# Kernel optimization log

Measured on AMD Instinct MI355X. Metric: run time of the kernel, lower is better.

## Reference

```python
import jax, jax.numpy as jnp
import numpy as np

B, T, C, H = 4, 4096, 1024, 64

def setup_inputs() -> dict:
    key = jax.random.key(0)
    kx, kk, kq, kv = jax.random.split(key, 4)
    x = jax.random.normal(kx, (B, T, C), dtype=jnp.float32)
    # causal lower-triangular mask; masked_fill where mask == 0
    mask = jnp.tril(jnp.ones((T, T), dtype=jnp.int32))
    s = 1.0 / np.sqrt(C)
    Wk = jax.random.normal(kk, (H, C), dtype=jnp.float32) * s
    Wq = jax.random.normal(kq, (H, C), dtype=jnp.float32) * s
    Wv = jax.random.normal(kv, (H, C), dtype=jnp.float32) * s
    return {"x": x, "mask": mask, "Wk": Wk, "Wq": Wq, "Wv": Wv}

def reference(x, mask, Wk, Wq, Wv):
    # single-head attention; dropout is identity in eval mode
    scale = Wk.shape[0] ** -0.5  # head_size ** -0.5
    k = jnp.einsum('btc,hc->bth', x, Wk)  # [B,T,H]
    q = jnp.einsum('btc,hc->bth', x, Wq)
    v = jnp.einsum('btc,hc->bth', x, Wv)
    att = jnp.einsum('bqh,bkh->bqk', q, k) * scale  # [B,T,T]
    att = jnp.where(mask == 0, -jnp.inf, att)
    att = jax.nn.softmax(att, axis=-1)
    out = jnp.einsum('bqk,bkh->bqh', att, v)  # [B,T,H]
    return out
```

## Files before the change

kernel.cpp:

```cpp
#include <hip/hip_runtime.h>
#include <hip/hip_bf16.h>

#define BT 16384
#define CDIM 1024
#define HD 64
#define TT 4096

typedef __bf16 bf16x8 __attribute__((ext_vector_type(8)));
typedef __bf16 bf16x4 __attribute__((ext_vector_type(4)));
typedef float f32x4 __attribute__((ext_vector_type(4)));

__device__ __forceinline__ f32x4 mfma16(bf16x8 a, bf16x8 b, f32x4 c){
  return __builtin_amdgcn_mfma_f32_16x16x32_bf16(a, b, c, 0, 0, 0);
}

__device__ __forceinline__ void glds16(const __bf16* g, __bf16* l){
  __builtin_amdgcn_global_load_lds(
      (const __attribute__((address_space(1))) unsigned int*)g,
      (__attribute__((address_space(3))) unsigned int*)l, 16, 0, 0);
}

__global__ __launch_bounds__(256) void wconv_k(const float* __restrict__ Wk,
    const float* __restrict__ Wq, const float* __restrict__ Wv,
    __bf16* __restrict__ Wbf){
  int idx = blockIdx.x*256 + threadIdx.x;
  int e0 = idx*4;
  int n = e0 >> 10;
  int c = e0 & 1023;
  const float* src; float s;
  if (n < 64)      { src = Wk + (size_t)n*CDIM;       s = 1.0f;   }
  else if (n < 128){ src = Wq + (size_t)(n-64)*CDIM;  s = 0.125f; }
  else             { src = Wv + (size_t)(n-128)*CDIM; s = 1.0f;   }
  float4 v = *reinterpret_cast<const float4*>(src + c);
  __bf16* dst = Wbf + e0;
  dst[0]=(__bf16)(v.x*s); dst[1]=(__bf16)(v.y*s);
  dst[2]=(__bf16)(v.z*s); dst[3]=(__bf16)(v.w*s);
}

__global__ __launch_bounds__(256) void proj_k(const float* __restrict__ x,
    const __bf16* __restrict__ Wbf, __bf16* __restrict__ kb,
    __bf16* __restrict__ qb, __bf16* __restrict__ vTb){
  __shared__ __bf16 Wt[2][192*64];
  __shared__ __bf16 Xt[2][32*64];

  const int tid  = threadIdx.x;
  const int lane = tid & 63;
  const int w    = tid >> 6;
  const int wr   = w >> 1;
  const int wn   = w & 1;
  const int l15  = lane & 15, g = lane >> 4;
  const long row0 = (long)blockIdx.x*32;

  const int xrw  = tid >> 3, xc16 = tid & 7;
  const float* xsrc = x + (row0 + xrw)*CDIM + xc16*8;
  const int    xdst = xrw*64 + ((xc16 ^ (xrw & 7))*8);

  const int swz0 = ((g    ) ^ (l15 & 7))*8;
  const int swz1 = ((g + 4) ^ (l15 & 7))*8;

  f32x4 acc[6];
  #pragma unroll
  for (int j=0;j<6;j++) acc[j] = (f32x4)(0.0f);

  float4 xlo, xhi;

  #pragma unroll
  for (int j=0;j<6;j++){
    const int s  = j*256 + w*64 + lane;
    const int rw = s >> 3, c16 = s & 7;
    glds16(Wbf + (size_t)rw*CDIM + ((c16 ^ (rw & 7))*8),
           &Wt[0][(j*256 + w*64)*8]);
  }
  xlo = *reinterpret_cast<const float4*>(xsrc);
  xhi = *reinterpret_cast<const float4*>(xsrc + 4);
  {
    bf16x8 xv;
    xv[0]=(__bf16)xlo.x; xv[1]=(__bf16)xlo.y; xv[2]=(__bf16)xlo.z; xv[3]=(__bf16)xlo.w;
    xv[4]=(__bf16)xhi.x; xv[5]=(__bf16)xhi.y; xv[6]=(__bf16)xhi.z; xv[7]=(__bf16)xhi.w;
    *reinterpret_cast<bf16x8*>(&Xt[0][xdst]) = xv;
  }
  xlo = *reinterpret_cast<const float4*>(xsrc + 64);
  xhi = *reinterpret_cast<const float4*>(xsrc + 64 + 4);
  asm volatile("s_waitcnt lgkmcnt(0)" ::: "memory");
  __builtin_amdgcn_sched_barrier(0);
  __builtin_amdgcn_s_barrier();
  __builtin_amdgcn_sched_barrier(0);

  #pragma unroll
  for (int t=0; t<16; ++t){
    const int cur = t & 1, nxt = cur ^ 1;

    if (t+1 < 16){
      const int kk0 = (t+1)*64;
      #pragma unroll
      for (int j=0;j<6;j++){
        const int s  = j*256 + w*64 + lane;
        const int rw = s >> 3, c16 = s & 7;
        glds16(Wbf + (size_t)rw*CDIM + kk0 + ((c16 ^ (rw & 7))*8),
               &Wt[nxt][(j*256 + w*64)*8]);
      }
    }
    if (t+1 < 16){
      bf16x8 xv;
      xv[0]=(__bf16)xlo.x; xv[1]=(__bf16)xlo.y; xv[2]=(__bf16)xlo.z; xv[3]=(__bf16)xlo.w;
      xv[4]=(__bf16)xhi.x; xv[5]=(__bf16)xhi.y; xv[6]=(__bf16)xhi.z; xv[7]=(__bf16)xhi.w;
      *reinterpret_cast<bf16x8*>(&Xt[nxt][xdst]) = xv;
    }
    if (t+2 < 16){
      const int nk = (t+2)*64;
      xlo = *reinterpret_cast<const float4*>(xsrc + nk);
      xhi = *reinterpret_cast<const float4*>(xsrc + nk + 4);
    }
    {
      const __bf16* ab = &Xt[cur][(wr*16 + l15)*64];
      bf16x8 a0 = *reinterpret_cast<const bf16x8*>(ab + swz0);
      bf16x8 a1 = *reinterpret_cast<const bf16x8*>(ab + swz1);
      const __bf16* bb = &Wt[cur][(wn*96 + l15)*64];
      #pragma unroll
      for (int nf=0; nf<6; ++nf){
        bf16x8 b0 = *reinterpret_cast<const bf16x8*>(bb + nf*1024 + swz0);
        bf16x8 b1 = *reinterpret_cast<const bf16x8*>(bb + nf*1024 + swz1);
        acc[nf] = mfma16(a1, b1, mfma16(a0, b0, acc[nf]));
      }
    }
    if (t+1 < 16){
      if (t+2 < 16){
        asm volatile("s_waitcnt vmcnt(2)" ::: "memory");
      } else {
        asm volatile("s_waitcnt vmcnt(0)" ::: "memory");
      }
      asm volatile("s_waitcnt lgkmcnt(0)" ::: "memory");
      __builtin_amdgcn_sched_barrier(0);
      __builtin_amdgcn_s_barrier();
      __builtin_amdgcn_sched_barrier(0);
    }
  }

  const long bidx = row0 >> 12;
  #pragma unroll
  for (int nf=0;nf<6;nf++){
    const int n0  = wn*96 + nf*16 + l15;
    const int mat = n0 >> 6;
    const int h   = n0 & 63;
    const long rbase = row0 + wr*16 + g*4;
    if (mat == 0){
      #pragma unroll
      for (int r=0;r<4;r++) kb[(rbase+r)*HD + h] = (__bf16)acc[nf][r];
    } else if (mat == 1){
      #pragma unroll
      for (int r=0;r<4;r++) qb[(rbase+r)*HD + h] = (__bf16)acc[nf][r];
    } else {
      bf16x4 t4;
      #pragma unroll
      for (int r=0;r<4;r++) t4[r] = (__bf16)acc[nf][r];
      *reinterpret_cast<bf16x4*>(vTb + (bidx*64 + h)*TT + (rbase & 4095)) = t4;
    }
  }
}

template<int NS>
__global__ __launch_bounds__(256) void attn_part_k(const __bf16* __restrict__ kbg,
    const __bf16* __restrict__ qbg, const __bf16* __restrict__ vT,
    __bf16* __restrict__ po, float* __restrict__ pl){
  __shared__ __bf16 Klds[64][72];
  __shared__ __bf16 Vlds[64][72];
  __shared__ __bf16 Plds[4][16][72];

  const int tid  = threadIdx.x;
  const int lane = tid & 63;
  const int w    = tid >> 6;
  const int l15  = lane & 15, g = lane >> 4;

  const int bi  = blockIdx.x;
  const int b   = bi / (64*NS);
  const int rem = bi % (64*NS);
  const int qt  = 63 - rem / NS;
  const int s   = rem % NS;

  const int ntiles = qt + 1;
  const int lo = ( s      * ntiles) / NS;
  const int hi = ((s + 1) * ntiles) / NS;
  const int pidx = (b*64 + qt)*NS + s;

  if (lo == hi){
    if (l15 == 0){
      #pragma unroll
      for (int r=0;r<4;r++) pl[pidx*64 + w*16 + g*4 + r] = 0.0f;
    }
    return;
  }

  const long qbase = (long)b*TT + (long)qt*64;

  bf16x8 qf0, qf1;
  {
    const __bf16* src = qbg + (qbase + w*16 + l15)*HD + g*8;
    qf0 = *reinterpret_cast<const bf16x8*>(src);
    qf1 = *reinterpret_cast<const bf16x8*>(src + 32);
  }

  f32x4 o[4];
  #pragma unroll
  for (int ch=0; ch<4; ++ch) o[ch] = (f32x4)(0.0f);
  float lp[4] = {0.f, 0.f, 0.f, 0.f};

  const __bf16* vbase = vT + (size_t)b*64*TT;

  const int skey = tid >> 2;
  const int sd0  = (tid & 3) * 16;
  bf16x8 kr0, kr1, vr0, vr1;

  {
    const long kvbase = (long)b*TT + (long)lo*64;
    const __bf16* ks = kbg + (kvbase + skey)*HD + sd0;
    kr0 = *reinterpret_cast<const bf16x8*>(ks);
    kr1 = *reinterpret_cast<const bf16x8*>(ks+8);
    const __bf16* vs = vbase + (size_t)skey*TT + lo*64 + sd0;
    vr0 = *reinterpret_cast<const bf16x8*>(vs);
    vr1 = *reinterpret_cast<const bf16x8*>(vs+8);
  }

  for (int kv=lo; kv<hi; ++kv){
    __syncthreads();
    *reinterpret_cast<bf16x8*>(&Klds[skey][sd0])   = kr0;
    *reinterpret_cast<bf16x8*>(&Klds[skey][sd0+8]) = kr1;
    *reinterpret_cast<bf16x8*>(&Vlds[skey][sd0])   = vr0;
    *reinterpret_cast<bf16x8*>(&Vlds[skey][sd0+8]) = vr1;
    __syncthreads();

    if (kv+1 < hi){
      const long nbase = (long)b*TT + (long)(kv+1)*64;
      const __bf16* ks = kbg + (nbase + skey)*HD + sd0;
      kr0 = *reinterpret_cast<const bf16x8*>(ks);
      kr1 = *reinterpret_cast<const bf16x8*>(ks+8);
      const __bf16* vs = vbase + (size_t)skey*TT + (kv+1)*64 + sd0;
      vr0 = *reinterpret_cast<const bf16x8*>(vs);
      vr1 = *reinterpret_cast<const bf16x8*>(vs+8);
    }

    f32x4 sv[4];
    __builtin_amdgcn_s_setprio(1);
    #pragma unroll
    for (int c=0;c<4;c++){
      bf16x8 kb0 = *reinterpret_cast<const bf16x8*>(&Klds[c*16 + l15][g*8]);
      bf16x8 kb1 = *reinterpret_cast<const bf16x8*>(&Klds[c*16 + l15][g*8 + 32]);
      sv[c] = mfma16(qf0, kb0, (f32x4)(-16.0f));
      sv[c] = mfma16(qf1, kb1, sv[c]);
    }
    __builtin_amdgcn_s_setprio(0);

    if (kv == qt){
      #pragma unroll
      for (int c=0;c<4;c++){
        const int key = c*16 + l15;
        #pragma unroll
        for (int r=0;r<4;r++){
          const int qr = w*16 + g*4 + r;
          if (key > qr) sv[c][r] = -1e30f;
        }
      }
    }

    #pragma unroll
    for (int c=0;c<4;c++){
      #pragma unroll
      for (int r=0;r<4;r++) sv[c][r] = __expf(sv[c][r]);
    }
    #pragma unroll
    for (int r=0;r<4;r++)
      lp[r] += (sv[0][r] + sv[1][r]) + (sv[2][r] + sv[3][r]);

    #pragma unroll
    for (int c=0;c<4;c++){
      #pragma unroll
      for (int r=0;r<4;r++) Plds[w][g*4+r][c*16 + l15] = (__bf16)sv[c][r];
    }
    asm volatile("s_waitcnt lgkmcnt(0)" ::: "memory");
    __builtin_amdgcn_sched_barrier(0);
    bf16x8 pa0 = *reinterpret_cast<const bf16x8*>(&Plds[w][l15][g*8]);
    bf16x8 pa1 = *reinterpret_cast<const bf16x8*>(&Plds[w][l15][g*8 + 32]);

    __builtin_amdgcn_s_setprio(1);
    #pragma unroll
    for (int ch=0; ch<4; ++ch){
      bf16x8 vb0 = *reinterpret_cast<const bf16x8*>(&Vlds[ch*16 + l15][g*8]);
      bf16x8 vb1 = *reinterpret_cast<const bf16x8*>(&Vlds[ch*16 + l15][g*8 + 32]);
      o[ch] = mfma16(pa0, vb0, o[ch]);
      o[ch] = mfma16(pa1, vb1, o[ch]);
    }
    __builtin_amdgcn_s_setprio(0);
  }

  float lr[4];
  #pragma unroll
  for (int r=0;r<4;r++){
    float v = lp[r];
    v += __shfl_xor(v, 1);
    v += __shfl_xor(v, 2);
    v += __shfl_xor(v, 4);
    v += __shfl_xor(v, 8);
    lr[r] = v;
  }
  float rl[4];
  #pragma unroll
  for (int r=0;r<4;r++) rl[r] = (lr[r] > 0.0f) ? 1.0f/lr[r] : 0.0f;

  __bf16* podst = po + (size_t)pidx*4096;
  #pragma unroll
  for (int ch=0; ch<4; ++ch){
    #pragma unroll
    for (int r=0;r<4;r++)
      podst[(w*16 + g*4 + r)*64 + ch*16 + l15] = (__bf16)(o[ch][r] * rl[r]);
  }
  if (l15 == 0){
    #pragma unroll
    for (int r=0;r<4;r++) pl[pidx*64 + w*16 + g*4 + r] = lr[r];
  }
}

template<int NS>
__global__ __launch_bounds__(256) void comb_k(const __bf16* __restrict__ po,
    const float* __restrict__ pl, float* __restrict__ out){
  const int idx   = blockIdx.x*256 + threadIdx.x;
  const int qrow  = idx >> 6;
  const int dim   = idx & 63;
  const int qtg   = qrow >> 6;
  const int rowin = qrow & 63;

  float num = 0.0f, den = 0.0f;
  #pragma unroll
  for (int s=0;s<NS;s++){
    const float l = pl[(qtg*NS + s)*64 + rowin];
    den += l;
    num += l * (float)po[(size_t)(qtg*NS + s)*4096 + rowin*64 + dim];
  }
  out[idx] = num / den;
}

extern "C" void kernel_launch(void* const* d_in, const int* in_sizes, int n_in,
                              void* d_out, int out_size, void* d_ws, size_t ws_size,
                              hipStream_t stream) {
  const float* x  = (const float*)d_in[0];
  const float* Wk = (const float*)d_in[2];
  const float* Wq = (const float*)d_in[3];
  const float* Wv = (const float*)d_in[4];
  float* out = (float*)d_out;

  char* ws = (char*)d_ws;
  __bf16* Wbf = (__bf16*)ws;
  __bf16* kb  = (__bf16*)(ws + 393216);
  __bf16* qb  = (__bf16*)(ws + 2490368);
  __bf16* vTb = (__bf16*)(ws + 4587520);
  __bf16* po  = (__bf16*)(ws + 6684672);

  wconv_k<<<192, 256, 0, stream>>>(Wk, Wq, Wv, Wbf);
  proj_k <<<512, 256, 0, stream>>>(x, Wbf, kb, qb, vTb);

  const size_t need8 = 6684672ull + (size_t)2048*4096*2 + (size_t)2048*64*4;
  if (ws_size >= need8){
    float* pl = (float*)(ws + 6684672 + (size_t)2048*4096*2);
    attn_part_k<8><<<2048, 256, 0, stream>>>(kb, qb, vTb, po, pl);
    comb_k<8>    <<<4096, 256, 0, stream>>>(po, pl, out);
  } else {
    float* pl = (float*)(ws + 6684672 + (size_t)1024*4096*2);
    attn_part_k<4><<<1024, 256, 0, stream>>>(kb, qb, vTb, po, pl);
    comb_k<4>    <<<4096, 256, 0, stream>>>(po, pl, out);
  }
}
```

Measured before the change: 62.60 us.

## Widen attention blocks to 128 query rows with 8 waves sharing K/V tiles

The split-KV attention kernel now processes 128 query rows per block with 512 threads (8 waves), so each K/V tile loaded into LDS is reused by twice as many query rows. The split count drops to a fixed 4, with 512 blocks in place of 2048. Waves whose rows lie entirely above a key tile skip it, and the diagonal mask is generalized. The combine kernel and workspace layout are adapted to match. This halves K/V global traffic per query row but reduces the number of blocks and adds causal imbalance across waves within a block.

```diff
diff --git a/kernel.cpp b/kernel.cpp
--- a/kernel.cpp
+++ b/kernel.cpp
@@ -5,6 +5,7 @@
 #define CDIM 1024
 #define HD 64
 #define TT 4096
+#define NS2 4
 
 typedef __bf16 bf16x8 __attribute__((ext_vector_type(8)));
 typedef __bf16 bf16x4 __attribute__((ext_vector_type(4)));
@@ -158,13 +159,12 @@
   }
 }
 
-template<int NS>
-__global__ __launch_bounds__(256) void attn_part_k(const __bf16* __restrict__ kbg,
+__global__ __launch_bounds__(512) void attn_part_k(const __bf16* __restrict__ kbg,
     const __bf16* __restrict__ qbg, const __bf16* __restrict__ vT,
     __bf16* __restrict__ po, float* __restrict__ pl){
   __shared__ __bf16 Klds[64][72];
   __shared__ __bf16 Vlds[64][72];
-  __shared__ __bf16 Plds[4][16][72];
+  __shared__ __bf16 Plds[8][16][72];
 
   const int tid  = threadIdx.x;
   const int lane = tid & 63;
@@ -172,25 +172,25 @@
   const int l15  = lane & 15, g = lane >> 4;
 
   const int bi  = blockIdx.x;
-  const int b   = bi / (64*NS);
-  const int rem = bi % (64*NS);
-  const int qt  = 63 - rem / NS;
-  const int s   = rem % NS;
-
-  const int ntiles = qt + 1;
-  const int lo = ( s      * ntiles) / NS;
-  const int hi = ((s + 1) * ntiles) / NS;
-  const int pidx = (b*64 + qt)*NS + s;
+  const int b   = bi / (32*NS2);
+  const int rem = bi % (32*NS2);
+  const int qt  = 31 - rem / NS2;
+  const int s   = rem % NS2;
+
+  const int ntiles = 2*qt + 2;
+  const int lo = ( s      * ntiles) / NS2;
+  const int hi = ((s + 1) * ntiles) / NS2;
+  const int pidx = (b*32 + qt)*NS2 + s;
 
   if (lo == hi){
     if (l15 == 0){
       #pragma unroll
-      for (int r=0;r<4;r++) pl[pidx*64 + w*16 + g*4 + r] = 0.0f;
+      for (int r=0;r<4;r++) pl[pidx*128 + w*16 + g*4 + r] = 0.0f;
     }
     return;
   }
 
-  const long qbase = (long)b*TT + (long)qt*64;
+  const long qbase = (long)b*TT + (long)qt*128;
 
   bf16x8 qf0, qf1;
   {
@@ -206,37 +206,30 @@
 
   const __bf16* vbase = vT + (size_t)b*64*TT;
 
-  const int skey = tid >> 2;
-  const int sd0  = (tid & 3) * 16;
-  bf16x8 kr0, kr1, vr0, vr1;
+  const int skey = tid >> 3;
+  const int sd0  = (tid & 7) * 8;
+  bf16x8 kr, vr;
 
   {
     const long kvbase = (long)b*TT + (long)lo*64;
-    const __bf16* ks = kbg + (kvbase + skey)*HD + sd0;
-    kr0 = *reinterpret_cast<const bf16x8*>(ks);
-    kr1 = *reinterpret_cast<const bf16x8*>(ks+8);
-    const __bf16* vs = vbase + (size_t)skey*TT + lo*64 + sd0;
-    vr0 = *reinterpret_cast<const bf16x8*>(vs);
-    vr1 = *reinterpret_cast<const bf16x8*>(vs+8);
+    kr = *reinterpret_cast<const bf16x8*>(kbg + (kvbase + skey)*HD + sd0);
+    vr = *reinterpret_cast<const bf16x8*>(vbase + (size_t)skey*TT + lo*64 + sd0);
   }
 
   for (int kv=lo; kv<hi; ++kv){
     __syncthreads();
-    *reinterpret_cast<bf16x8*>(&Klds[skey][sd0])   = kr0;
-    *reinterpret_cast<bf16x8*>(&Klds[skey][sd0+8]) = kr1;
-    *reinterpret_cast<bf16x8*>(&Vlds[skey][sd0])   = vr0;
-    *reinterpret_cast<bf16x8*>(&Vlds[skey][sd0+8]) = vr1;
+    *reinterpret_cast<bf16x8*>(&Klds[skey][sd0]) = kr;
+    *reinterpret_cast<bf16x8*>(&Vlds[skey][sd0]) = vr;
     __syncthreads();
 
     if (kv+1 < hi){
       const long nbase = (long)b*TT + (long)(kv+1)*64;
-      const __bf16* ks = kbg + (nbase + skey)*HD + sd0;
-      kr0 = *reinterpret_cast<const bf16x8*>(ks);
-      kr1 = *reinterpret_cast<const bf16x8*>(ks+8);
-      const __bf16* vs = vbase + (size_t)skey*TT + (kv+1)*64 + sd0;
-      vr0 = *reinterpret_cast<const bf16x8*>(vs);
-      vr1 = *reinterpret_cast<const bf16x8*>(vs+8);
-    }
+      kr = *reinterpret_cast<const bf16x8*>(kbg + (nbase + skey)*HD + sd0);
+      vr = *reinterpret_cast<const bf16x8*>(vbase + (size_t)skey*TT + (kv+1)*64 + sd0);
+    }
+
+    const int kk0 = kv*64 - qt*128;
+    if (kk0 > w*16 + 15) continue;
 
     f32x4 sv[4];
     __builtin_amdgcn_s_setprio(1);
@@ -249,14 +242,14 @@
     }
     __builtin_amdgcn_s_setprio(0);
 
-    if (kv == qt){
+    if (kk0 + 63 > w*16){
       #pragma unroll
       for (int c=0;c<4;c++){
-        const int key = c*16 + l15;
+        const int key_rel = kk0 + c*16 + l15;
         #pragma unroll
         for (int r=0;r<4;r++){
-          const int qr = w*16 + g*4 + r;
-          if (key > qr) sv[c][r] = -1e30f;
+          const int row_rel = w*16 + g*4 + r;
+          if (key_rel > row_rel) sv[c][r] = -1e30f;
         }
       }
     }
@@ -305,7 +298,7 @@
   #pragma unroll
   for (int r=0;r<4;r++) rl[r] = (lr[r] > 0.0f) ? 1.0f/lr[r] : 0.0f;
 
-  __bf16* podst = po + (size_t)pidx*4096;
+  __bf16* podst = po + (size_t)pidx*8192;
   #pragma unroll
   for (int ch=0; ch<4; ++ch){
     #pragma unroll
@@ -314,25 +307,24 @@
   }
   if (l15 == 0){
     #pragma unroll
-    for (int r=0;r<4;r++) pl[pidx*64 + w*16 + g*4 + r] = lr[r];
-  }
-}
-
-template<int NS>
+    for (int r=0;r<4;r++) pl[pidx*128 + w*16 + g*4 + r] = lr[r];
+  }
+}
+
 __global__ __launch_bounds__(256) void comb_k(const __bf16* __restrict__ po,
     const float* __restrict__ pl, float* __restrict__ out){
   const int idx   = blockIdx.x*256 + threadIdx.x;
   const int qrow  = idx >> 6;
   const int dim   = idx & 63;
-  const int qtg   = qrow >> 6;
-  const int rowin = qrow & 63;
+  const int qtg   = qrow >> 7;
+  const int rowin = qrow & 127;
 
   float num = 0.0f, den = 0.0f;
   #pragma unroll
-  for (int s=0;s<NS;s++){
-    const float l = pl[(qtg*NS + s)*64 + rowin];
+  for (int s=0;s<NS2;s++){
+    const float l = pl[(qtg*NS2 + s)*128 + rowin];
     den += l;
-    num += l * (float)po[(size_t)(qtg*NS + s)*4096 + rowin*64 + dim];
+    num += l * (float)po[(size_t)(qtg*NS2 + s)*8192 + rowin*64 + dim];
   }
   out[idx] = num / den;
 }
@@ -352,18 +344,10 @@
   __bf16* qb  = (__bf16*)(ws + 2490368);
   __bf16* vTb = (__bf16*)(ws + 4587520);
   __bf16* po  = (__bf16*)(ws + 6684672);
-
-  wconv_k<<<192, 256, 0, stream>>>(Wk, Wq, Wv, Wbf);
-  proj_k <<<512, 256, 0, stream>>>(x, Wbf, kb, qb, vTb);
-
-  const size_t need8 = 6684672ull + (size_t)2048*4096*2 + (size_t)2048*64*4;
-  if (ws_size >= need8){
-    float* pl = (float*)(ws + 6684672 + (size_t)2048*4096*2);
-    attn_part_k<8><<<2048, 256, 0, stream>>>(kb, qb, vTb, po, pl);
-    comb_k<8>    <<<4096, 256, 0, stream>>>(po, pl, out);
-  } else {
-    float* pl = (float*)(ws + 6684672 + (size_t)1024*4096*2);
-    attn_part_k<4><<<1024, 256, 0, stream>>>(kb, qb, vTb, po, pl);
-    comb_k<4>    <<<4096, 256, 0, stream>>>(po, pl, out);
-  }
-}
+  float*  pl  = (float*)(ws + 15073280);
+
+  wconv_k    <<<192, 256, 0, stream>>>(Wk, Wq, Wv, Wbf);
+  proj_k     <<<512, 256, 0, stream>>>(x, Wbf, kb, qb, vTb);
+  attn_part_k<<<512, 512, 0, stream>>>(kb, qb, vTb, po, pl);
+  comb_k     <<<4096, 256, 0, stream>>>(po, pl, out);
+}
```

Result: slower. 67.16 us (+7.3%).
